# Optimization experiments

Measured on AMD Instinct MI355X. Metric: run time of the kernel, lower is better.

Reference implementation:

```python
import jax, jax.numpy as jnp
import numpy as np

N = 100000
E = 1600000
IN_DIM = 128
HID = 128
OUT = 8


def _linear_params(key, fan_in, fan_out, bias=True):
    k1, k2 = jax.random.split(key)
    bound = 1.0 / np.sqrt(fan_in)
    W = jax.random.uniform(k1, (fan_in, fan_out), jnp.float32, -bound, bound)
    if bias:
        b = jax.random.uniform(k2, (fan_out,), jnp.float32, -bound, bound)
        return W, b
    return W


def setup_inputs() -> dict:
    key = jax.random.key(0)
    ks = jax.random.split(key, 20)
    x = jax.random.normal(ks[0], (N, IN_DIM), jnp.float32)
    edge_index = jax.random.randint(ks[1], (2, E), 0, N, jnp.int64)
    y = jax.random.randint(ks[2], (N,), 0, 2, jnp.int64)
    pmp_mask = jax.random.randint(ks[3], (N,), 0, 2, jnp.int64).astype(jnp.bool_)
    # layer 1 params
    W_fr1 = _linear_params(ks[4], IN_DIM, HID, bias=False)
    W_be1 = _linear_params(ks[5], IN_DIM, HID, bias=False)
    alpha_w1, alpha_b1 = _linear_params(ks[6], IN_DIM, 1)
    Wself_w1, Wself_b1 = _linear_params(ks[7], IN_DIM, HID)
    # layer 2 params
    W_fr2 = _linear_params(ks[8], HID, HID, bias=False)
    W_be2 = _linear_params(ks[9], HID, HID, bias=False)
    alpha_w2, alpha_b2 = _linear_params(ks[10], HID, 1)
    Wself_w2, Wself_b2 = _linear_params(ks[11], HID, HID)
    # classifier
    cls_w, cls_b = _linear_params(ks[12], HID, OUT)
    return dict(x=x, edge_index=edge_index, y=y, pmp_mask=pmp_mask,
                W_fr1=W_fr1, W_be1=W_be1, alpha_w1=alpha_w1, alpha_b1=alpha_b1,
                Wself_w1=Wself_w1, Wself_b1=Wself_b1,
                W_fr2=W_fr2, W_be2=W_be2, alpha_w2=alpha_w2, alpha_b2=alpha_b2,
                Wself_w2=Wself_w2, Wself_b2=Wself_b2,
                cls_w=cls_w, cls_b=cls_b)


def _pmp_layer(x, src, dst, node_type, W_fr, W_be, alpha_w, alpha_b, Wself_w, Wself_b):
    # alpha_mlp: Linear(in,1) -> sigmoid, per node
    alpha = jax.nn.sigmoid(x @ alpha_w + alpha_b)          # [N,1]
    xj = x[src]                                            # gather source feats [E,d]
    msg_fr = xj @ W_fr                                     # [E,h]
    msg_be = xj @ W_be                                     # [E,h]
    a = alpha[dst]                                         # gather target alpha [E,1]
    ntj = node_type[src][:, None]                          # [E,1]
    msg_un = a * msg_fr + (1.0 - a) * msg_be
    msg = jnp.where(ntj == 1, msg_fr, jnp.where(ntj == 0, msg_be, msg_un))
    aggr = jax.ops.segment_sum(msg, dst, num_segments=N)   # scatter-add into targets
    return aggr + x @ Wself_w + Wself_b


def reference(x, edge_index, y, pmp_mask,
              W_fr1, W_be1, alpha_w1, alpha_b1, Wself_w1, Wself_b1,
              W_fr2, W_be2, alpha_w2, alpha_b2, Wself_w2, Wself_b2,
              cls_w, cls_b):
    src, dst = edge_index[0], edge_index[1]  # PyG: row=source j, col=target i
    node_type = jnp.where(pmp_mask, y, jnp.full_like(y, 2))  # [N], in {0,1,2}
    h = _pmp_layer(x, src, dst, node_type, W_fr1, W_be1, alpha_w1, alpha_b1, Wself_w1, Wself_b1)
    h = jax.nn.relu(h)
    # dropout inactive (inference)
    h = _pmp_layer(h, src, dst, node_type, W_fr2, W_be2, alpha_w2, alpha_b2, Wself_w2, Wself_b2)
    h = jax.nn.relu(h)
    return h @ cls_w + cls_b
```

## Files before the change

### kernel.cpp

```cpp
#include <hip/hip_runtime.h>
#include <hip/hip_bf16.h>
#include <cmath>

#define DEV static __device__ __forceinline__

constexpr int NN = 100000;
constexpr int NN_PAD = 100352;
constexpr int NE = 1600000;
constexpr int D  = 128;
constexpr int KTOT = 384;
constexpr int SCHUNK = 1024;
constexpr int NBS = (NN + SCHUNK - 1) / SCHUNK;

typedef __attribute__((ext_vector_type(8))) short short8;
typedef __attribute__((ext_vector_type(4))) float f32x4;

DEV float bf2f(unsigned short u) {
    unsigned int t = ((unsigned int)u) << 16;
    return __builtin_bit_cast(float, t);
}
DEV unsigned short f2bf(float f) {
    unsigned int u = __builtin_bit_cast(unsigned int, f);
    u += 0x7fffu + ((u >> 16) & 1u);
    return (unsigned short)(u >> 16);
}
DEV unsigned int packbf(float a, float b) {
    return (unsigned int)f2bf(a) | ((unsigned int)f2bf(b) << 16);
}

__global__ void k_detect(const unsigned int* __restrict__ ew,
                         const unsigned int* __restrict__ yw,
                         const unsigned int* __restrict__ mw,
                         int* __restrict__ flags) {
    int lane = threadIdx.x & 63;
    int c_e = __popcll(__ballot(ew[2 * lane + 1] != 0u));
    int c_y = __popcll(__ballot(yw[2 * lane + 1] != 0u));
    int c_mb = __popcll(__ballot(mw[lane] > 1u));
    int c_mz = __popcll(__ballot(mw[2 * lane + 1] != 0u));
    if (lane == 0) {
        flags[1] = (c_e < 8) ? 1 : 0;
        flags[2] = (c_y < 8) ? 1 : 0;
        flags[3] = c_mb > 8 ? 2 : (c_mz < 8 ? 1 : 0);
    }
}

__global__ void k_prep(const int* __restrict__ flg, const void* __restrict__ y,
                       const void* __restrict__ mask, int* __restrict__ nt) {
    int i = blockIdx.x * blockDim.x + threadIdx.x;
    if (i >= NN) return;
    int yv = flg[2] ? (int)((const long long*)y)[i] : ((const int*)y)[i];
    int mm = flg[3] == 2 ? (int)((const unsigned char*)mask)[i]
           : flg[3] == 1 ? (int)((const long long*)mask)[i]
           : ((const int*)mask)[i];
    nt[i] = mm ? yv : 2;
}

__global__ void k_conv_e(const int* __restrict__ flg, const void* __restrict__ ei,
                         const int* __restrict__ nt,
                         int* __restrict__ SP, int* __restrict__ DST,
                         int* __restrict__ deg, int* __restrict__ rnk) {
    int e = blockIdx.x * blockDim.x + threadIdx.x;
    if (e >= NE) return;
    int s, d;
    if (flg[1]) {
        const long long* p = (const long long*)ei;
        s = (int)p[e]; d = (int)p[NE + e];
    } else {
        const int* p = (const int*)ei;
        s = p[e]; d = p[NE + e];
    }
    SP[e] = (s << 2) | nt[s];
    DST[e] = d;
    rnk[e] = atomicAdd(&deg[d], 1);
}

__global__ void k_convx(const float* __restrict__ x,
                        unsigned short* __restrict__ Ahi, unsigned short* __restrict__ XLO) {
    long t = blockIdx.x * (long)blockDim.x + threadIdx.x;
    long g = t * 4;
    if (g >= (long)NN * D) return;
    int n = (int)(g >> 7);
    int k = (int)(g & 127);
    float4 v = *(const float4*)(x + g);
    float vv[4] = {v.x, v.y, v.z, v.w};
    ushort4 hi, lo;
    unsigned short* hp = (unsigned short*)&hi;
    unsigned short* lp = (unsigned short*)&lo;
#pragma unroll
    for (int j = 0; j < 4; j++) {
        unsigned short h = f2bf(vv[j]);
        hp[j] = h;
        lp[j] = f2bf(vv[j] - bf2f(h));
    }
    *(ushort4*)(Ahi + (size_t)n * KTOT + k) = hi;
    *(ushort4*)(XLO + (size_t)n * D + k) = lo;
}

__global__ void k_wprep(const float* __restrict__ Wsf, const float* __restrict__ Wfr,
                        const float* __restrict__ Wbe,
                        unsigned short* __restrict__ WpHi, unsigned short* __restrict__ WpLo) {
    int t = blockIdx.x * blockDim.x + threadIdx.x;
    if (t >= KTOT * D) return;
    int k = t >> 7;
    int c = t & 127;
    float w = k < 128 ? Wsf[k * 128 + c]
            : k < 256 ? Wfr[(k - 128) * 128 + c]
            : Wbe[(k - 256) * 128 + c];
    unsigned short hi = f2bf(w);
    unsigned short lo = f2bf(w - bf2f(hi));
    int kt = k >> 5, kin = k & 31;
    int grp = kin >> 3, j = kin & 7;
    int ct = c >> 4, cl = c & 15;
    size_t idx = (((size_t)kt * 8 + ct) * 64 + ((grp << 4) | cl)) * 8 + j;
    WpHi[idx] = hi;
    WpLo[idx] = lo;
}

__global__ void k_scan_a(const int* __restrict__ deg, int* __restrict__ bsum) {
    __shared__ int sh[256];
    int b = blockIdx.x, t = threadIdx.x;
    int base = b * SCHUNK + t * 4;
    int s = 0;
#pragma unroll
    for (int j = 0; j < 4; j++) { int i = base + j; if (i < NN) s += deg[i]; }
    sh[t] = s; __syncthreads();
    for (int d = 128; d > 0; d >>= 1) {
        if (t < d) sh[t] += sh[t + d];
        __syncthreads();
    }
    if (t == 0) bsum[b] = sh[0];
}

__global__ void k_scan_b(const int* __restrict__ bsum, int* __restrict__ bpre,
                         int* __restrict__ offs) {
    __shared__ int sh[128];
    int t = threadIdx.x;
    int v = (t < NBS) ? bsum[t] : 0;
    int incl = v; sh[t] = incl; __syncthreads();
    for (int d = 1; d < 128; d <<= 1) {
        int add = (t >= d) ? sh[t - d] : 0;
        __syncthreads();
        incl += add; sh[t] = incl;
        __syncthreads();
    }
    if (t < NBS) bpre[t] = incl - v;
    if (t == 0) offs[NN] = NE;
}

__global__ void k_scan_c(const int* __restrict__ deg, const int* __restrict__ bpre,
                         int* __restrict__ offs) {
    __shared__ int sh[256];
    int b = blockIdx.x, t = threadIdx.x;
    int base = b * SCHUNK + t * 4;
    int v[4];
#pragma unroll
    for (int j = 0; j < 4; j++) { int i = base + j; v[j] = (i < NN) ? deg[i] : 0; }
    int tsum = v[0] + v[1] + v[2] + v[3];
    int incl = tsum; sh[t] = incl; __syncthreads();
    for (int d = 1; d < 256; d <<= 1) {
        int add = (t >= d) ? sh[t - d] : 0;
        __syncthreads();
        incl += add; sh[t] = incl;
        __syncthreads();
    }
    int ex = (incl - tsum) + bpre[b];
#pragma unroll
    for (int j = 0; j < 4; j++) {
        int i = base + j;
        if (i < NN) { offs[i] = ex; ex += v[j]; }
    }
}

__global__ void k_place(const int* __restrict__ SP, const int* __restrict__ DST,
                        const int* __restrict__ RNK, const int* __restrict__ offs,
                        int* __restrict__ ssrc) {
    for (int e = blockIdx.x * blockDim.x + threadIdx.x; e < NE; e += gridDim.x * blockDim.x) {
        int d = DST[e];
        int slot = offs[d] + RNK[e];
        __builtin_nontemporal_store(SP[e], &ssrc[slot]);
    }
}

__global__ void __launch_bounds__(256)
k_aggr(unsigned short* __restrict__ Ahi, const unsigned short* __restrict__ XLO,
       const int* __restrict__ sp, const int* __restrict__ offs,
       const float* __restrict__ aw, const float* __restrict__ ab) {
    int lane = threadIdx.x & 63;
    int d = blockIdx.x * (blockDim.x >> 6) + (threadIdx.x >> 6);
    if (d >= NN) return;
    int eg = lane >> 4;
    int dg = lane & 15;
    int k0 = dg * 8;

    int ak = lane * 2;
    unsigned int whi = *(const unsigned int*)(Ahi + (size_t)d * KTOT + ak);
    unsigned int wlo = *(const unsigned int*)(XLO + (size_t)d * D + ak);
    float xa = bf2f((unsigned short)(whi & 0xffffu)) + bf2f((unsigned short)(wlo & 0xffffu));
    float xb = bf2f((unsigned short)(whi >> 16)) + bf2f((unsigned short)(wlo >> 16));
    float dot = xa * aw[ak] + xb * aw[ak + 1];
#pragma unroll
    for (int m = 32; m > 0; m >>= 1) dot += __shfl_xor(dot, m, 64);
    float a = 1.0f / (1.0f + expf(-(dot + ab[0])));
    float oma = 1.0f - a;

    float u[8], v[8];
#pragma unroll
    for (int q = 0; q < 8; q++) { u[q] = 0.f; v[q] = 0.f; }

    int e0 = offs[d];
    int n = offs[d + 1] - e0;
    const int* spp = sp + e0;
    for (int base = 0; base < n; base += 8) {
        int iA = base + eg;
        int iB = base + 4 + eg;
        int cA = iA < n ? iA : 0;
        int cB = iB < n ? iB : 0;
        int pkA = spp[cA];
        int pkB = spp[cB];
        int bA = pkA & 3, sA = pkA >> 2;
        int bB = pkB & 3, sB = pkB >> 2;
        float cuA = iA < n ? ((bA == 1) ? 1.f : (bA == 0 ? 0.f : a)) : 0.f;
        float cvA = iA < n ? ((bA == 0) ? 1.f : (bA == 1 ? 0.f : oma)) : 0.f;
        float cuB = iB < n ? ((bB == 1) ? 1.f : (bB == 0 ? 0.f : a)) : 0.f;
        float cvB = iB < n ? ((bB == 0) ? 1.f : (bB == 1 ? 0.f : oma)) : 0.f;
        uint4 wA = *(const uint4*)(Ahi + (size_t)sA * KTOT + k0);
        uint4 wB = *(const uint4*)(Ahi + (size_t)sB * KTOT + k0);
        const unsigned int* wa = (const unsigned int*)&wA;
        const unsigned int* wb = (const unsigned int*)&wB;
#pragma unroll
        for (int q = 0; q < 4; q++) {
            float a0 = bf2f((unsigned short)(wa[q] & 0xffffu));
            float a1 = bf2f((unsigned short)(wa[q] >> 16));
            float b0 = bf2f((unsigned short)(wb[q] & 0xffffu));
            float b1 = bf2f((unsigned short)(wb[q] >> 16));
            u[2 * q]     += cuA * a0 + cuB * b0;
            u[2 * q + 1] += cuA * a1 + cuB * b1;
            v[2 * q]     += cvA * a0 + cvB * b0;
            v[2 * q + 1] += cvA * a1 + cvB * b1;
        }
    }

#pragma unroll
    for (int q = 0; q < 8; q++) {
        u[q] += __shfl_xor(u[q], 16, 64);
        u[q] += __shfl_xor(u[q], 32, 64);
        v[q] += __shfl_xor(v[q], 16, 64);
        v[q] += __shfl_xor(v[q], 32, 64);
    }
    if (eg == 0) {
        unsigned int up[4], vp[4];
#pragma unroll
        for (int q = 0; q < 4; q++) {
            up[q] = packbf(u[2 * q], u[2 * q + 1]);
            vp[q] = packbf(v[2 * q], v[2 * q + 1]);
        }
        *(uint4*)(Ahi + (size_t)d * KTOT + 128 + k0) = *(uint4*)up;
        *(uint4*)(Ahi + (size_t)d * KTOT + 256 + k0) = *(uint4*)vp;
    }
}

__global__ void __launch_bounds__(256)
k_mfma(unsigned short* __restrict__ Ahi, unsigned short* __restrict__ XLO,
       const unsigned short* __restrict__ WpHi, const unsigned short* __restrict__ WpLo,
       const float* __restrict__ bias) {
    int lane = threadIdx.x & 63;
    int wave = threadIdx.x >> 6;
    int r0 = blockIdx.x * 256 + wave * 64;

    int mrow = lane & 15, kgrp = lane >> 4;
    const unsigned short* aHiB = Ahi + (size_t)(r0 + mrow) * KTOT + kgrp * 8;
    const unsigned short* aLoB = XLO + (size_t)(r0 + mrow) * D + kgrp * 8;

    f32x4 acc[4][8];
#pragma unroll
    for (int m = 0; m < 4; m++)
#pragma unroll
        for (int i = 0; i < 8; i++) acc[m][i] = (f32x4){0.f, 0.f, 0.f, 0.f};

#pragma unroll
    for (int kt = 0; kt < 12; kt++) {
        short8 ah[4], al[4];
#pragma unroll
        for (int m = 0; m < 4; m++) {
            ah[m] = *(const short8*)(aHiB + (size_t)m * 16 * KTOT + kt * 32);
            if (kt < 4) al[m] = *(const short8*)(aLoB + (size_t)m * 16 * D + kt * 32);
        }
#pragma unroll
        for (int ct = 0; ct < 8; ct++) {
            size_t wb = (((size_t)kt * 8 + ct) * 64 + lane) * 8;
            short8 bh = *(const short8*)(WpHi + wb);
            short8 bl = *(const short8*)(WpLo + wb);
#pragma unroll
            for (int m = 0; m < 4; m++) {
                acc[m][ct] = __builtin_amdgcn_mfma_f32_16x16x32_bf16(ah[m], bh, acc[m][ct], 0, 0, 0);
                acc[m][ct] = __builtin_amdgcn_mfma_f32_16x16x32_bf16(ah[m], bl, acc[m][ct], 0, 0, 0);
                if (kt < 4)
                    acc[m][ct] = __builtin_amdgcn_mfma_f32_16x16x32_bf16(al[m], bh, acc[m][ct], 0, 0, 0);
            }
        }
    }

    int ccol = lane & 15;
#pragma unroll
    for (int m = 0; m < 4; m++) {
        int crow = r0 + m * 16 + (lane >> 4) * 4;
#pragma unroll
        for (int ct = 0; ct < 8; ct++) {
            float bb = bias[ct * 16 + ccol];
#pragma unroll
            for (int r = 0; r < 4; r++) {
                float v = fmaxf(acc[m][ct][r] + bb, 0.f);
                unsigned short h = f2bf(v);
                unsigned short l = f2bf(v - bf2f(h));
                Ahi[(size_t)(crow + r) * KTOT + ct * 16 + ccol] = h;
                XLO[(size_t)(crow + r) * D + ct * 16 + ccol] = l;
            }
        }
    }
}

__global__ void __launch_bounds__(256)
k_cls(const unsigned short* __restrict__ Ahi, const unsigned short* __restrict__ XLO,
      const float* __restrict__ W, const float* __restrict__ b, float* __restrict__ out) {
    int lane = threadIdx.x & 63;
    int wid = blockIdx.x * (blockDim.x >> 6) + (threadIdx.x >> 6);
    if (wid >= NN) return;
    int cc = lane & 7;
    int kg = lane >> 3;
    const unsigned short* hH = Ahi + (size_t)wid * KTOT + kg * 16;
    const unsigned short* hL = XLO + (size_t)wid * D + kg * 16;
    float s = 0.f;
#pragma unroll
    for (int j = 0; j < 16; j += 2) {
        unsigned int ph = *(const unsigned int*)(hH + j);
        unsigned int pl = *(const unsigned int*)(hL + j);
        float h0 = bf2f((unsigned short)(ph & 0xffffu)) + bf2f((unsigned short)(pl & 0xffffu));
        float h1 = bf2f((unsigned short)(ph >> 16)) + bf2f((unsigned short)(pl >> 16));
        s += h0 * W[(kg * 16 + j) * 8 + cc];
        s += h1 * W[(kg * 16 + j + 1) * 8 + cc];
    }
    s += __shfl_xor(s, 8, 64);
    s += __shfl_xor(s, 16, 64);
    s += __shfl_xor(s, 32, 64);
    if (lane < 8) out[(size_t)wid * 8 + cc] = s + b[cc];
}

extern "C" void kernel_launch(void* const* d_in, const int* in_sizes, int n_in,
                              void* d_out, int out_size, void* d_ws, size_t ws_size,
                              hipStream_t stream) {
    const float* x   = (const float*)d_in[0];
    const void* ei   = d_in[1];
    const void* y    = d_in[2];
    const void* mask = d_in[3];

    char* ws = (char*)d_ws;
    size_t cur_off = 0;
    auto alloc = [&](size_t bytes) {
        size_t o = cur_off;
        cur_off = (cur_off + bytes + 255) & ~(size_t)255;
        return o;
    };

    size_t oAhi = alloc((size_t)NN_PAD * KTOT * 2);
    size_t oXLO = alloc((size_t)NN_PAD * D * 2);
    size_t oW1h = alloc(KTOT * D * 2);
    size_t oW1l = alloc(KTOT * D * 2);
    size_t oW2h = alloc(KTOT * D * 2);
    size_t oW2l = alloc(KTOT * D * 2);
    size_t oNT   = alloc(NN * 4);
    size_t oDEG  = alloc(NN * 4);
    size_t oOFFS = alloc((NN + 1) * 4);
    size_t oBSUM = alloc(NBS * 4);
    size_t oBPRE = alloc(NBS * 4);
    size_t oSP   = alloc((size_t)NE * 4);
    size_t oDST  = alloc((size_t)NE * 4);
    size_t oRNK  = alloc((size_t)NE * 4);
    size_t oSSRC = alloc((size_t)NE * 4);
    size_t oFLG  = alloc(256);

    unsigned short* Ahi = (unsigned short*)(ws + oAhi);
    unsigned short* XLO = (unsigned short*)(ws + oXLO);
    unsigned short* W1h = (unsigned short*)(ws + oW1h);
    unsigned short* W1l = (unsigned short*)(ws + oW1l);
    unsigned short* W2h = (unsigned short*)(ws + oW2h);
    unsigned short* W2l = (unsigned short*)(ws + oW2l);
    int* NT   = (int*)(ws + oNT);
    int* DEG  = (int*)(ws + oDEG);
    int* OFFS = (int*)(ws + oOFFS);
    int* BSUM = (int*)(ws + oBSUM);
    int* BPRE = (int*)(ws + oBPRE);
    int* SP   = (int*)(ws + oSP);
    int* DST  = (int*)(ws + oDST);
    int* RNK  = (int*)(ws + oRNK);
    int* SSRC = (int*)(ws + oSSRC);
    int* FLG  = (int*)(ws + oFLG);

    hipMemsetAsync(DEG, 0, NN * sizeof(int), stream);

    k_detect<<<1, 64, 0, stream>>>((const unsigned int*)ei, (const unsigned int*)y,
                                   (const unsigned int*)mask, FLG);
    k_prep<<<(NN + 255) / 256, 256, 0, stream>>>(FLG, y, mask, NT);
    k_conv_e<<<(NE + 255) / 256, 256, 0, stream>>>(FLG, ei, NT, SP, DST, DEG, RNK);
    k_convx<<<NN * D / 4 / 256, 256, 0, stream>>>(x, Ahi, XLO);
    k_wprep<<<(KTOT * D + 255) / 256, 256, 0, stream>>>(
        (const float*)d_in[8], (const float*)d_in[4], (const float*)d_in[5], W1h, W1l);
    k_wprep<<<(KTOT * D + 255) / 256, 256, 0, stream>>>(
        (const float*)d_in[14], (const float*)d_in[10], (const float*)d_in[11], W2h, W2l);

    k_scan_a<<<NBS, 256, 0, stream>>>(DEG, BSUM);
    k_scan_b<<<1, 128, 0, stream>>>(BSUM, BPRE, OFFS);
    k_scan_c<<<NBS, 256, 0, stream>>>(DEG, BPRE, OFFS);
    k_place<<<2048, 256, 0, stream>>>(SP, DST, RNK, OFFS, SSRC);

    k_aggr<<<NN / 4, 256, 0, stream>>>(Ahi, XLO, SSRC, OFFS,
        (const float*)d_in[6], (const float*)d_in[7]);
    k_mfma<<<NN_PAD / 256, 256, 0, stream>>>(Ahi, XLO, W1h, W1l, (const float*)d_in[9]);
    k_aggr<<<NN / 4, 256, 0, stream>>>(Ahi, XLO, SSRC, OFFS,
        (const float*)d_in[12], (const float*)d_in[13]);
    k_mfma<<<NN_PAD / 256, 256, 0, stream>>>(Ahi, XLO, W2h, W2l, (const float*)d_in[15]);

    k_cls<<<NN / 4, 256, 0, stream>>>(Ahi, XLO, (const float*)d_in[16],
                                      (const float*)d_in[17], (float*)d_out);
}
```

Baseline: 496.6 us.

## Stage MFMA weight tiles in double-buffered LDS and halve rows per wave

The dense MFMA kernel now copies each k-tile of the packed hi/lo bf16 weights into a double-buffered shared-memory buffer, so all four waves read weights from LDS instead of each fetching them from global memory. Each wave now covers 32 rows instead of 64, so twice as many blocks are launched. This cuts redundant global weight traffic and the accumulator register count, which may raise occupancy. In exchange it adds a block-wide barrier per k-tile and halves A-operand reuse of each weight fragment per wave.

```diff
diff --git a/kernel.cpp b/kernel.cpp
--- a/kernel.cpp
+++ b/kernel.cpp
@@ -263,46 +263,67 @@
 k_mfma(unsigned short* __restrict__ Ahi, unsigned short* __restrict__ XLO,
        const unsigned short* __restrict__ WpHi, const unsigned short* __restrict__ WpLo,
        const float* __restrict__ bias) {
-    int lane = threadIdx.x & 63;
-    int wave = threadIdx.x >> 6;
-    int r0 = blockIdx.x * 256 + wave * 64;
+    __shared__ unsigned short ldsB[2][2][4096];
+    int t = threadIdx.x;
+    int lane = t & 63;
+    int wave = t >> 6;
+    int r0 = blockIdx.x * 128 + wave * 32;
 
     int mrow = lane & 15, kgrp = lane >> 4;
     const unsigned short* aHiB = Ahi + (size_t)(r0 + mrow) * KTOT + kgrp * 8;
     const unsigned short* aLoB = XLO + (size_t)(r0 + mrow) * D + kgrp * 8;
 
-    f32x4 acc[4][8];
-#pragma unroll
-    for (int m = 0; m < 4; m++)
+    f32x4 acc[2][8];
+#pragma unroll
+    for (int m = 0; m < 2; m++)
 #pragma unroll
         for (int i = 0; i < 8; i++) acc[m][i] = (f32x4){0.f, 0.f, 0.f, 0.f};
 
+    {
+        int o = t * 8;
+        *(uint4*)&ldsB[0][0][o]        = *(const uint4*)(WpHi + o);
+        *(uint4*)&ldsB[0][0][o + 2048] = *(const uint4*)(WpHi + o + 2048);
+        *(uint4*)&ldsB[0][1][o]        = *(const uint4*)(WpLo + o);
+        *(uint4*)&ldsB[0][1][o + 2048] = *(const uint4*)(WpLo + o + 2048);
+    }
+    __syncthreads();
+
+    int buf = 0;
 #pragma unroll
     for (int kt = 0; kt < 12; kt++) {
-        short8 ah[4], al[4];
-#pragma unroll
-        for (int m = 0; m < 4; m++) {
+        if (kt < 11) {
+            int src = (kt + 1) * 4096 + t * 8;
+            int o = t * 8;
+            *(uint4*)&ldsB[buf ^ 1][0][o]        = *(const uint4*)(WpHi + src);
+            *(uint4*)&ldsB[buf ^ 1][0][o + 2048] = *(const uint4*)(WpHi + src + 2048);
+            *(uint4*)&ldsB[buf ^ 1][1][o]        = *(const uint4*)(WpLo + src);
+            *(uint4*)&ldsB[buf ^ 1][1][o + 2048] = *(const uint4*)(WpLo + src + 2048);
+        }
+        short8 ah[2], al[2];
+#pragma unroll
+        for (int m = 0; m < 2; m++) {
             ah[m] = *(const short8*)(aHiB + (size_t)m * 16 * KTOT + kt * 32);
             if (kt < 4) al[m] = *(const short8*)(aLoB + (size_t)m * 16 * D + kt * 32);
         }
 #pragma unroll
         for (int ct = 0; ct < 8; ct++) {
-            size_t wb = (((size_t)kt * 8 + ct) * 64 + lane) * 8;
-            short8 bh = *(const short8*)(WpHi + wb);
-            short8 bl = *(const short8*)(WpLo + wb);
-#pragma unroll
-            for (int m = 0; m < 4; m++) {
+            short8 bh = *(const short8*)&ldsB[buf][0][ct * 512 + lane * 8];
+            short8 bl = *(const short8*)&ldsB[buf][1][ct * 512 + lane * 8];
+#pragma unroll
+            for (int m = 0; m < 2; m++) {
                 acc[m][ct] = __builtin_amdgcn_mfma_f32_16x16x32_bf16(ah[m], bh, acc[m][ct], 0, 0, 0);
                 acc[m][ct] = __builtin_amdgcn_mfma_f32_16x16x32_bf16(ah[m], bl, acc[m][ct], 0, 0, 0);
                 if (kt < 4)
                     acc[m][ct] = __builtin_amdgcn_mfma_f32_16x16x32_bf16(al[m], bh, acc[m][ct], 0, 0, 0);
             }
         }
+        __syncthreads();
+        buf ^= 1;
     }
 
     int ccol = lane & 15;
 #pragma unroll
-    for (int m = 0; m < 4; m++) {
+    for (int m = 0; m < 2; m++) {
         int crow = r0 + m * 16 + (lane >> 4) * 4;
 #pragma unroll
         for (int ct = 0; ct < 8; ct++) {
@@ -414,10 +435,10 @@
 
     k_aggr<<<NN / 4, 256, 0, stream>>>(Ahi, XLO, SSRC, OFFS,
         (const float*)d_in[6], (const float*)d_in[7]);
-    k_mfma<<<NN_PAD / 256, 256, 0, stream>>>(Ahi, XLO, W1h, W1l, (const float*)d_in[9]);
+    k_mfma<<<NN_PAD / 128, 256, 0, stream>>>(Ahi, XLO, W1h, W1l, (const float*)d_in[9]);
     k_aggr<<<NN / 4, 256, 0, stream>>>(Ahi, XLO, SSRC, OFFS,
         (const float*)d_in[12], (const float*)d_in[13]);
-    k_mfma<<<NN_PAD / 256, 256, 0, stream>>>(Ahi, XLO, W2h, W2l, (const float*)d_in[15]);
+    k_mfma<<<NN_PAD / 128, 256, 0, stream>>>(Ahi, XLO, W2h, W2l, (const float*)d_in[15]);
 
     k_cls<<<NN / 4, 256, 0, stream>>>(Ahi, XLO, (const float*)d_in[16],
                                       (const float*)d_in[17], (float*)d_out);
```

Measured after the change: 461.3 us. 7.1% less time.
